# Kernel tuning notes

Measured on AMD Instinct MI355X. Metric: run time of the kernel, lower is better.

The kernel has to match this reference:

```python
import jax, jax.numpy as jnp
import numpy as np

NUM_HEADS = 16
HEAD_DIM = 64
EMBED_DIM = 1024
MASKED_BIAS = -10000.0


def setup_inputs() -> dict:
    key = jax.random.key(0)
    ks = jax.random.split(key, 4)
    B, S, D = 4, 1024, EMBED_DIM
    scale = 0.02
    return {
        "hidden_states": jax.random.normal(ks[0], (B, S, D), dtype=jnp.float32),
        "c_attn_w": jax.random.normal(ks[1], (D, 3 * D), dtype=jnp.float32) * scale,
        "c_attn_b": jnp.zeros((3 * D,), dtype=jnp.float32),
        "c_proj_w": jax.random.normal(ks[2], (D, D), dtype=jnp.float32) * scale,
        "c_proj_b": jnp.zeros((D,), dtype=jnp.float32),
        "affine_w": jnp.ones((D,), dtype=jnp.float32),
        "affine_b": jnp.zeros((D,), dtype=jnp.float32),
    }


def reference(hidden_states, c_attn_w, c_attn_b, c_proj_w, c_proj_b, affine_w, affine_b):
    B, S, D = hidden_states.shape
    H, Dh = NUM_HEADS, HEAD_DIM
    # c_attn (GPT2 Conv1D): x @ W + b -> [B,S,3D], split into q,k,v
    qkv = hidden_states @ c_attn_w + c_attn_b
    q, k, v = jnp.split(qkv, 3, axis=-1)
    # split heads -> [B,H,S,Dh]
    def split_heads(t):
        return t.reshape(B, S, H, Dh).transpose(0, 2, 1, 3)
    q, k, v = split_heads(q), split_heads(k), split_heads(v)
    # QK^T scaled by 1/sqrt(head_dim) (value.size(-1)**0.5)
    attn_weights = jnp.einsum("bhqd,bhkd->bhqk", q, k) / jnp.asarray(
        Dh, hidden_states.dtype) ** 0.5
    # causal mask via where with -10000 sentinel (eager GPT2 semantics)
    causal = jnp.tril(jnp.ones((S, S), dtype=bool))[None, None]
    attn_weights = jnp.where(causal, attn_weights,
                             jnp.asarray(MASKED_BIAS, attn_weights.dtype))
    attn_weights = jax.nn.softmax(attn_weights, axis=-1)
    # attn dropout = identity in eval
    attn_output = jnp.einsum("bhqk,bhkd->bhqd", attn_weights, v)
    # merge heads -> [B,S,D]
    attn_output = attn_output.transpose(0, 2, 1, 3).reshape(B, S, D)
    # c_proj (Conv1D), resid dropout identity, then affine
    attn_output = attn_output @ c_proj_w + c_proj_b
    attn_output = attn_output * affine_w + affine_b
    return attn_output
```

## Files before the change

kernel.cpp:

```cpp
#include <hip/hip_runtime.h>


typedef __attribute__((ext_vector_type(4))) float  fx4;
typedef __attribute__((ext_vector_type(4))) short  sx4;
typedef __attribute__((ext_vector_type(8))) short  sx8;
typedef __attribute__((ext_vector_type(4))) float  f32x4;
typedef __attribute__((ext_vector_type(8))) __bf16 bf16x8;

#define DEVI static __device__ __forceinline__

DEVI short f2bf(float f) {
  unsigned u = __builtin_bit_cast(unsigned, f);
  u = (u + 0x7FFFu + ((u >> 16) & 1u)) >> 16;
  return (short)u;
}

DEVI fx4 mfma16(sx8 a, sx8 b, fx4 c) {
  return __builtin_amdgcn_mfma_f32_16x16x32_bf16(
      __builtin_bit_cast(bf16x8, a), __builtin_bit_cast(bf16x8, b), c, 0, 0, 0);
}

DEVI void gl_lds16(const void* g, void* l) {
  __builtin_amdgcn_global_load_lds(
      (const __attribute__((address_space(1))) void*)g,
      (__attribute__((address_space(3))) void*)l, 16, 0, 0);
}

__global__ __launch_bounds__(256) void cast_bf16(const float* __restrict__ in,
                                                 short* __restrict__ out, int n4) {
  int i = blockIdx.x * blockDim.x + threadIdx.x;
  if (i < n4) {
    f32x4 v = *(const f32x4*)&in[(size_t)i * 4];
    sx4 o;
#pragma unroll
    for (int j = 0; j < 4; ++j) o[j] = f2bf(v[j]);
    *(sx4*)&out[(size_t)i * 4] = o;
  }
}

__global__ __launch_bounds__(256) void transpose_bf16(const float* __restrict__ in,
                                                      short* __restrict__ out,
                                                      int R, int C) {
  __shared__ float t[32][33];
  int tx = threadIdx.x & 31, ty = threadIdx.x >> 5;
  int r0 = blockIdx.y * 32, c0 = blockIdx.x * 32;
#pragma unroll
  for (int i = 0; i < 4; ++i)
    t[ty + i * 8][tx] = in[(size_t)(r0 + ty + i * 8) * C + c0 + tx];
  __syncthreads();
#pragma unroll
  for (int i = 0; i < 4; ++i)
    out[(size_t)(c0 + ty + i * 8) * R + r0 + tx] = f2bf(t[tx][ty + i * 8]);
}

__global__ __launch_bounds__(512, 2) void gemm_qkv(
    const short* __restrict__ A, const short* __restrict__ Bt,
    const float* __restrict__ bias, short* __restrict__ Qg,
    short* __restrict__ Kg, short* __restrict__ Vtg) {
  __shared__ __align__(16) short As[2][256][32];
  __shared__ __align__(16) short Bs[2][256][32];
  const int tid = threadIdx.x, lane = tid & 63, w = tid >> 6;
  const int bid = blockIdx.x;
  const int x = bid & 7, k = bid >> 3;
  const int bm = (x & 3) * 4 + (k & 3);
  const int bn = (x >> 2) * 6 + (k >> 2);
  const int wm = w >> 2, wn = w & 3;
  const int c0 = lane & 15, g = lane >> 4;
  const int lr16 = lane >> 2;
  const int xs = (lr16 ^ (lr16 >> 2)) & 3;
  const int src_slot = (lane & 3) ^ xs;
  const int K = 1024;
  fx4 acc[8][4] = {};

  auto STAGE = [&](int bf, int kt) {
#pragma unroll
    for (int i = 0; i < 2; ++i) {
      int ch = w * 2 + i;
      int row = ch * 16 + lr16;
      gl_lds16(&A[(size_t)(bm * 256 + row) * K + kt + src_slot * 8], &As[bf][ch * 16][0]);
      gl_lds16(&Bt[(size_t)(bn * 256 + row) * K + kt + src_slot * 8], &Bs[bf][ch * 16][0]);
    }
  };

  STAGE(0, 0);
  for (int t = 0; t < 32; ++t) {
    const int bf = t & 1;
    if (t + 1 < 32) {
      STAGE(bf ^ 1, (t + 1) * 32);
      asm volatile("s_waitcnt vmcnt(4)" ::: "memory");
    } else {
      asm volatile("s_waitcnt vmcnt(0)" ::: "memory");
    }
    __builtin_amdgcn_s_barrier();

    sx8 af[8], bfr[4];
#pragma unroll
    for (int m = 0; m < 8; ++m) {
      int row = wm * 128 + m * 16 + c0;
      af[m] = *(const sx8*)&As[bf][row][(g ^ ((row ^ (row >> 2)) & 3)) * 8];
    }
#pragma unroll
    for (int n = 0; n < 4; ++n) {
      int row = wn * 64 + n * 16 + c0;
      bfr[n] = *(const sx8*)&Bs[bf][row][(g ^ ((row ^ (row >> 2)) & 3)) * 8];
    }
    __builtin_amdgcn_s_setprio(1);
#pragma unroll
    for (int m = 0; m < 8; ++m)
#pragma unroll
      for (int n = 0; n < 4; ++n) acc[m][n] = mfma16(af[m], bfr[n], acc[m][n]);
    __builtin_amdgcn_s_setprio(0);
    __builtin_amdgcn_s_barrier();
  }

  const float SCALE_Q = 0.125f * 1.4426950408889634f;
#pragma unroll
  for (int m = 0; m < 8; ++m) {
#pragma unroll
    for (int n = 0; n < 4; ++n) {
      int col = bn * 256 + wn * 64 + n * 16 + c0;
      int row0 = bm * 256 + wm * 128 + m * 16 + g * 4;
      float bv = bias[col];
      int b = row0 >> 10, s0 = row0 & 1023;
      if (col < 1024) {
        int h = col >> 6, d = col & 63;
        size_t base = ((size_t)(b * 16 + h) * 1024) * 64 + d;
#pragma unroll
        for (int r = 0; r < 4; ++r)
          Qg[base + (size_t)(s0 + r) * 64] = f2bf((acc[m][n][r] + bv) * SCALE_Q);
      } else if (col < 2048) {
        int c = col - 1024, h = c >> 6, d = c & 63;
        size_t base = ((size_t)(b * 16 + h) * 1024) * 64 + d;
#pragma unroll
        for (int r = 0; r < 4; ++r)
          Kg[base + (size_t)(s0 + r) * 64] = f2bf(acc[m][n][r] + bv);
      } else {
        int c = col - 2048, h = c >> 6, d = c & 63;
        sx4 v;
#pragma unroll
        for (int r = 0; r < 4; ++r) v[r] = f2bf(acc[m][n][r] + bv);
        *(sx4*)&Vtg[((size_t)(b * 16 + h) * 64 + d) * 1024 + s0] = v;
      }
    }
  }
}

__global__ __launch_bounds__(512, 4) void gemm_proj(
    const short* __restrict__ A, const short* __restrict__ Bt,
    const float* __restrict__ bias, const float* __restrict__ aw,
    const float* __restrict__ ab, float* __restrict__ Out) {
  __shared__ __align__(16) short As[2][128][64];
  __shared__ __align__(16) short Bs[2][128][64];
  const int tid = threadIdx.x, lane = tid & 63, w = tid >> 6;
  const int bid = blockIdx.x;
  const int x = bid & 7, k = bid >> 3;
  const int bn = x, bm = k;
  const int wm = w >> 2, wn = w & 3;
  const int c0 = lane & 15, g = lane >> 4;
  const int lr8 = lane >> 3, ls8 = (lane & 7) ^ lr8;
  const int K = 1024, N = 1024;
  fx4 acc[4][2] = {};

  auto STAGE = [&](int bf, int kt) {
#pragma unroll
    for (int i = 0; i < 2; ++i) {
      int idx = w * 2 + i;
      gl_lds16(&A[(size_t)(bm * 128 + idx * 8 + lr8) * K + kt + ls8 * 8],
               &As[bf][idx * 8][0]);
      gl_lds16(&Bt[(size_t)(bn * 128 + idx * 8 + lr8) * K + kt + ls8 * 8],
               &Bs[bf][idx * 8][0]);
    }
  };

  STAGE(0, 0);
  for (int t = 0; t < 16; ++t) {
    const int bf = t & 1;
    if (t + 1 < 16) {
      STAGE(bf ^ 1, (t + 1) * 64);
      asm volatile("s_waitcnt vmcnt(4)" ::: "memory");
    } else {
      asm volatile("s_waitcnt vmcnt(0)" ::: "memory");
    }
    __builtin_amdgcn_s_barrier();
    __builtin_amdgcn_s_setprio(1);
#pragma unroll
    for (int kk = 0; kk < 2; ++kk) {
      sx8 af[4], bfr[2];
      int sb = kk * 4 + g;
#pragma unroll
      for (int m = 0; m < 4; ++m) {
        int row = wm * 64 + m * 16 + c0;
        af[m] = *(const sx8*)&As[bf][row][(sb ^ (row & 7)) * 8];
      }
#pragma unroll
      for (int n = 0; n < 2; ++n) {
        int row = wn * 32 + n * 16 + c0;
        bfr[n] = *(const sx8*)&Bs[bf][row][(sb ^ (row & 7)) * 8];
      }
#pragma unroll
      for (int m = 0; m < 4; ++m)
#pragma unroll
        for (int n = 0; n < 2; ++n) acc[m][n] = mfma16(af[m], bfr[n], acc[m][n]);
    }
    __builtin_amdgcn_s_setprio(0);
    __builtin_amdgcn_s_barrier();
  }

#pragma unroll
  for (int m = 0; m < 4; ++m) {
#pragma unroll
    for (int n = 0; n < 2; ++n) {
      int col = bn * 128 + wn * 32 + n * 16 + c0;
      int row0 = bm * 128 + wm * 64 + m * 16 + g * 4;
      float bv = bias[col], wv = aw[col], av = ab[col];
#pragma unroll
      for (int r = 0; r < 4; ++r)
        Out[(size_t)(row0 + r) * N + col] = (acc[m][n][r] + bv) * wv + av;
    }
  }
}

__global__ __launch_bounds__(256, 4) void attn_kernel(const short* __restrict__ Qg,
                                                      const short* __restrict__ Kg,
                                                      const short* __restrict__ Vtg,
                                                      short* __restrict__ AO) {
  __shared__ __align__(16) short Ks[2][64][64];
  __shared__ __align__(16) short Vts[2][64][64];
  __shared__ __align__(16) short Ps[4][16 * 64];
  const int tid = threadIdx.x, lane = tid & 63, w = tid >> 6;
  const int bid = blockIdx.x;
  const int u = bid >> 8, v = bid & 255, bh = v >> 2, jj = v & 3;
  const int qt = (u == 0) ? jj : (u == 1) ? 7 - jj : (u == 2) ? 8 + jj : 15 - jj;
  const int b = bh >> 4, h = bh & 15;
  const int c0 = lane & 15, g = lane >> 4;
  const int lr8 = lane >> 3, ls8 = (lane & 7) ^ lr8;
  const int q0 = qt * 64 + w * 16;
  const short* Qp = Qg + (size_t)bh * 65536;
  const short* Kp = Kg + (size_t)bh * 65536;
  const short* Vp = Vtg + (size_t)bh * 65536;
  short* pbase = &Ps[w][0];
  const int s8 = (c0 & 7) * 8;

  sx8 qf[2];
#pragma unroll
  for (int kk = 0; kk < 2; ++kk)
    qf[kk] = *(const sx8*)&Qp[(size_t)(q0 + c0) * 64 + kk * 32 + g * 8];

  fx4 o[4] = {};
  float mrun = -1e30f, lrun = 0.f;
  const int q_glob = q0 + c0;

  auto STAGE = [&](int bf, int kv0) {
#pragma unroll
    for (int i = 0; i < 2; ++i) {
      int idx = w * 2 + i;
      gl_lds16(&Kp[(size_t)(kv0 + idx * 8 + lr8) * 64 + ls8 * 8], &Ks[bf][idx * 8][0]);
    }
#pragma unroll
    for (int i = 0; i < 2; ++i) {
      int idx = w * 2 + i;
      gl_lds16(&Vp[(size_t)(idx * 8 + lr8) * 1024 + kv0 + ls8 * 8], &Vts[bf][idx * 8][0]);
    }
  };

  STAGE(0, 0);
  for (int t = 0; t <= qt; ++t) {
    const int kv0 = t * 64;
    const int bf = t & 1;
    const bool more = t < qt;
    if (more) {
      STAGE(bf ^ 1, kv0 + 64);
      asm volatile("s_waitcnt vmcnt(4)" ::: "memory");
    } else {
      asm volatile("s_waitcnt vmcnt(0)" ::: "memory");
    }
    __builtin_amdgcn_s_barrier();

    fx4 st[4];
    __builtin_amdgcn_s_setprio(1);
#pragma unroll
    for (int mf = 0; mf < 4; ++mf) {
      int row = mf * 16 + c0;
      sx8 kf0 = *(const sx8*)&Ks[bf][row][(g ^ (row & 7)) * 8];
      sx8 kf1 = *(const sx8*)&Ks[bf][row][((4 + g) ^ (row & 7)) * 8];
      fx4 z = {0.f, 0.f, 0.f, 0.f};
      z = mfma16(kf0, qf[0], z);
      st[mf] = mfma16(kf1, qf[1], z);
    }
    __builtin_amdgcn_s_setprio(0);

    float pmax = -1e30f;
    if (t == qt) {
#pragma unroll
      for (int mf = 0; mf < 4; ++mf)
#pragma unroll
        for (int r = 0; r < 4; ++r) {
          int kv = kv0 + mf * 16 + g * 4 + r;
          float z = (kv > q_glob) ? -1e30f : st[mf][r];
          st[mf][r] = z;
          pmax = fmaxf(pmax, z);
        }
    } else {
#pragma unroll
      for (int mf = 0; mf < 4; ++mf)
#pragma unroll
        for (int r = 0; r < 4; ++r) pmax = fmaxf(pmax, st[mf][r]);
    }
    pmax = fmaxf(pmax, __shfl_xor(pmax, 16));
    pmax = fmaxf(pmax, __shfl_xor(pmax, 32));
    float mnew = fmaxf(mrun, pmax);
    float alpha = __builtin_amdgcn_exp2f(mrun - mnew);
    float psum = 0.f;
#pragma unroll
    for (int mf = 0; mf < 4; ++mf) {
      sx4 pv;
#pragma unroll
      for (int r = 0; r < 4; ++r) {
        float pp = __builtin_amdgcn_exp2f(st[mf][r] - mnew);
        psum += pp;
        pv[r] = f2bf(pp);
      }
      *(sx4*)&pbase[c0 * 64 + ((mf * 16 + g * 4) ^ s8)] = pv;
    }
    psum += __shfl_xor(psum, 16);
    psum += __shfl_xor(psum, 32);
    lrun = lrun * alpha + psum;
    mrun = mnew;
#pragma unroll
    for (int mf = 0; mf < 4; ++mf) o[mf] *= alpha;

    __builtin_amdgcn_s_setprio(1);
#pragma unroll
    for (int kk = 0; kk < 2; ++kk) {
      sx8 pbf = *(const sx8*)&pbase[c0 * 64 + ((kk * 32 + g * 8) ^ s8)];
#pragma unroll
      for (int mf = 0; mf < 4; ++mf) {
        int row = mf * 16 + c0;
        sx8 vaf = *(const sx8*)&Vts[bf][row][((kk * 4 + g) ^ (row & 7)) * 8];
        o[mf] = mfma16(vaf, pbf, o[mf]);
      }
    }
    __builtin_amdgcn_s_setprio(0);
    __builtin_amdgcn_s_barrier();
  }

  float inv = 1.0f / lrun;
  int q = q0 + c0;
#pragma unroll
  for (int mf = 0; mf < 4; ++mf) {
    sx4 v4;
#pragma unroll
    for (int r = 0; r < 4; ++r) v4[r] = f2bf(o[mf][r] * inv);
    int d0 = mf * 16 + g * 4;
    *(sx4*)&AO[((size_t)(b * 1024 + q)) * 1024 + h * 64 + d0] = v4;
  }
}

extern "C" void kernel_launch(void* const* d_in, const int* in_sizes, int n_in,
                              void* d_out, int out_size, void* d_ws, size_t ws_size,
                              hipStream_t stream) {
  const float* hs  = (const float*)d_in[0];
  const float* caw = (const float*)d_in[1];
  const float* cab = (const float*)d_in[2];
  const float* cpw = (const float*)d_in[3];
  const float* cpb = (const float*)d_in[4];
  const float* afw = (const float*)d_in[5];
  const float* afb = (const float*)d_in[6];
  float* out = (float*)d_out;
  char* ws = (char*)d_ws;

  short* hsb    = (short*)(ws);
  short* ao     = (short*)(ws);
  short* wqkvt  = (short*)(ws + ((size_t)8  << 20));
  short* wprojt = (short*)(ws + ((size_t)14 << 20));
  short* Qg     = (short*)(ws + ((size_t)16 << 20));
  short* Kg     = (short*)(ws + ((size_t)24 << 20));
  short* Vtg    = (short*)(ws + ((size_t)32 << 20));

  cast_bf16<<<4096, 256, 0, stream>>>(hs, hsb, 1048576);
  transpose_bf16<<<dim3(96, 32), 256, 0, stream>>>(caw, wqkvt, 1024, 3072);
  transpose_bf16<<<dim3(32, 32), 256, 0, stream>>>(cpw, wprojt, 1024, 1024);
  gemm_qkv<<<192, 512, 0, stream>>>(hsb, wqkvt, cab, Qg, Kg, Vtg);
  attn_kernel<<<1024, 256, 0, stream>>>(Qg, Kg, Vtg, ao);
  gemm_proj<<<256, 512, 0, stream>>>(ao, wprojt, cpb, afw, afb, out);
}
```

Measured before the change: 110.0 us.

## Shrink QKV GEMM tile to 128x256 with paired-row LDS swizzle and more blocks

The QKV projection GEMM now uses 128x256 output tiles instead of 256x256, doubling the grid to 384 blocks and halving the per-wave accumulators to raise occupancy (launch bounds 4). LDS tiles are re-laid out so that two 32-wide K rows pack into one 64-element row with an XOR swizzle, and the block-to-tile mapping is changed for the new grid. Barriers are switched to an inline-asm s_barrier with a memory clobber. The aim is better CU fill on 256 CUs, traded against more redundant loads of the B operand.

```diff
diff --git a/kernel.cpp b/kernel.cpp
--- a/kernel.cpp
+++ b/kernel.cpp
@@ -8,6 +8,7 @@
 typedef __attribute__((ext_vector_type(8))) __bf16 bf16x8;
 
 #define DEVI static __device__ __forceinline__
+#define BARRIER asm volatile("s_barrier" ::: "memory")
 
 DEVI short f2bf(float f) {
   unsigned u = __builtin_bit_cast(unsigned, f);
@@ -53,32 +54,35 @@
     out[(size_t)(c0 + ty + i * 8) * R + r0 + tx] = f2bf(t[tx][ty + i * 8]);
 }
 
-__global__ __launch_bounds__(512, 2) void gemm_qkv(
+__global__ __launch_bounds__(512, 4) void gemm_qkv(
     const short* __restrict__ A, const short* __restrict__ Bt,
     const float* __restrict__ bias, short* __restrict__ Qg,
     short* __restrict__ Kg, short* __restrict__ Vtg) {
-  __shared__ __align__(16) short As[2][256][32];
-  __shared__ __align__(16) short Bs[2][256][32];
+  __shared__ __align__(16) short As[2][64][64];
+  __shared__ __align__(16) short Bs[2][128][64];
   const int tid = threadIdx.x, lane = tid & 63, w = tid >> 6;
   const int bid = blockIdx.x;
-  const int x = bid & 7, k = bid >> 3;
-  const int bm = (x & 3) * 4 + (k & 3);
-  const int bn = (x >> 2) * 6 + (k >> 2);
+  const int x = bid & 7, loc = bid >> 3;
+  const int bn = (x & 3) * 3 + loc % 3;
+  const int bm = (x >> 2) * 16 + loc / 3;
   const int wm = w >> 2, wn = w & 3;
   const int c0 = lane & 15, g = lane >> 4;
-  const int lr16 = lane >> 2;
-  const int xs = (lr16 ^ (lr16 >> 2)) & 3;
-  const int src_slot = (lane & 3) ^ xs;
+  const int l3 = lane >> 3, l7 = lane & 7;
+  const int slog = l7 ^ l3;
+  const int par = slog >> 2, gg = slog & 3;
   const int K = 1024;
-  fx4 acc[8][4] = {};
+  fx4 acc[4][4] = {};
 
   auto STAGE = [&](int bf, int kt) {
+    {
+      int row = w * 16 + l3 * 2 + par;
+      gl_lds16(&A[(size_t)(bm * 128 + row) * K + kt + gg * 8], &As[bf][w * 8][0]);
+    }
 #pragma unroll
     for (int i = 0; i < 2; ++i) {
       int ch = w * 2 + i;
-      int row = ch * 16 + lr16;
-      gl_lds16(&A[(size_t)(bm * 256 + row) * K + kt + src_slot * 8], &As[bf][ch * 16][0]);
-      gl_lds16(&Bt[(size_t)(bn * 256 + row) * K + kt + src_slot * 8], &Bs[bf][ch * 16][0]);
+      int row = ch * 16 + l3 * 2 + par;
+      gl_lds16(&Bt[(size_t)(bn * 256 + row) * K + kt + gg * 8], &Bs[bf][ch * 8][0]);
     }
   };
 
@@ -87,39 +91,41 @@
     const int bf = t & 1;
     if (t + 1 < 32) {
       STAGE(bf ^ 1, (t + 1) * 32);
-      asm volatile("s_waitcnt vmcnt(4)" ::: "memory");
+      asm volatile("s_waitcnt vmcnt(3)" ::: "memory");
     } else {
       asm volatile("s_waitcnt vmcnt(0)" ::: "memory");
     }
-    __builtin_amdgcn_s_barrier();
-
-    sx8 af[8], bfr[4];
-#pragma unroll
-    for (int m = 0; m < 8; ++m) {
-      int row = wm * 128 + m * 16 + c0;
-      af[m] = *(const sx8*)&As[bf][row][(g ^ ((row ^ (row >> 2)) & 3)) * 8];
+    BARRIER;
+
+    sx8 af[4], bfr[4];
+#pragma unroll
+    for (int m = 0; m < 4; ++m) {
+      int r = wm * 64 + m * 16 + c0, pr = r >> 1;
+      int sl = (((r & 1) << 2) | g) ^ (pr & 7);
+      af[m] = *(const sx8*)&As[bf][pr][sl * 8];
     }
 #pragma unroll
     for (int n = 0; n < 4; ++n) {
-      int row = wn * 64 + n * 16 + c0;
-      bfr[n] = *(const sx8*)&Bs[bf][row][(g ^ ((row ^ (row >> 2)) & 3)) * 8];
+      int r = wn * 64 + n * 16 + c0, pr = r >> 1;
+      int sl = (((r & 1) << 2) | g) ^ (pr & 7);
+      bfr[n] = *(const sx8*)&Bs[bf][pr][sl * 8];
     }
     __builtin_amdgcn_s_setprio(1);
 #pragma unroll
-    for (int m = 0; m < 8; ++m)
+    for (int m = 0; m < 4; ++m)
 #pragma unroll
       for (int n = 0; n < 4; ++n) acc[m][n] = mfma16(af[m], bfr[n], acc[m][n]);
     __builtin_amdgcn_s_setprio(0);
-    __builtin_amdgcn_s_barrier();
+    BARRIER;
   }
 
   const float SCALE_Q = 0.125f * 1.4426950408889634f;
 #pragma unroll
-  for (int m = 0; m < 8; ++m) {
+  for (int m = 0; m < 4; ++m) {
 #pragma unroll
     for (int n = 0; n < 4; ++n) {
       int col = bn * 256 + wn * 64 + n * 16 + c0;
-      int row0 = bm * 256 + wm * 128 + m * 16 + g * 4;
+      int row0 = bm * 128 + wm * 64 + m * 16 + g * 4;
       float bv = bias[col];
       int b = row0 >> 10, s0 = row0 & 1023;
       if (col < 1024) {
@@ -181,7 +187,7 @@
     } else {
       asm volatile("s_waitcnt vmcnt(0)" ::: "memory");
     }
-    __builtin_amdgcn_s_barrier();
+    BARRIER;
     __builtin_amdgcn_s_setprio(1);
 #pragma unroll
     for (int kk = 0; kk < 2; ++kk) {
@@ -203,7 +209,7 @@
         for (int n = 0; n < 2; ++n) acc[m][n] = mfma16(af[m], bfr[n], acc[m][n]);
     }
     __builtin_amdgcn_s_setprio(0);
-    __builtin_amdgcn_s_barrier();
+    BARRIER;
   }
 
 #pragma unroll
@@ -274,7 +280,7 @@
     } else {
       asm volatile("s_waitcnt vmcnt(0)" ::: "memory");
     }
-    __builtin_amdgcn_s_barrier();
+    BARRIER;
 
     fx4 st[4];
     __builtin_amdgcn_s_setprio(1);
@@ -341,7 +347,7 @@
       }
     }
     __builtin_amdgcn_s_setprio(0);
-    __builtin_amdgcn_s_barrier();
+    BARRIER;
   }
 
   float inv = 1.0f / lrun;
@@ -380,7 +386,7 @@
   cast_bf16<<<4096, 256, 0, stream>>>(hs, hsb, 1048576);
   transpose_bf16<<<dim3(96, 32), 256, 0, stream>>>(caw, wqkvt, 1024, 3072);
   transpose_bf16<<<dim3(32, 32), 256, 0, stream>>>(cpw, wprojt, 1024, 1024);
-  gemm_qkv<<<192, 512, 0, stream>>>(hsb, wqkvt, cab, Qg, Kg, Vtg);
+  gemm_qkv<<<384, 512, 0, stream>>>(hsb, wqkvt, cab, Qg, Kg, Vtg);
   attn_kernel<<<1024, 256, 0, stream>>>(Qg, Kg, Vtg, ao);
   gemm_proj<<<256, 512, 0, stream>>>(ao, wprojt, cpb, afw, afb, out);
 }
```

Result: faster. 97.75 us (-11.1%).
